# Kernel tuning notes

Measured on AMD Instinct MI355X. Metric: run time of the kernel, lower is better.

The kernel has to match this reference:

```python
import jax, jax.numpy as jnp
import numpy as np

E = 1024  # embed_dim
H = 16    # num_heads
D = E // H  # head_dim
B, S = 2, 2048

def _xavier(key, shape):
    fan_in, fan_out = shape[1], shape[0]
    limit = float(np.sqrt(6.0 / (fan_in + fan_out)))
    return jax.random.uniform(key, shape, jnp.float32, -limit, limit)

def setup_inputs() -> dict:
    key = jax.random.key(0)
    ks = jax.random.split(key, 7)
    return {
        "query": jax.random.normal(ks[0], (B, S, E), jnp.float32),
        "key": jax.random.normal(ks[1], (B, S, E), jnp.float32),
        "value": jax.random.normal(ks[2], (B, S, E), jnp.float32),
        "Wq": _xavier(ks[3], (E, E)), "bq": jnp.zeros((E,), jnp.float32),
        "Wk": _xavier(ks[4], (E, E)), "bk": jnp.zeros((E,), jnp.float32),
        "Wv": _xavier(ks[5], (E, E)), "bv": jnp.zeros((E,), jnp.float32),
        "Wo": _xavier(ks[6], (E, E)), "bo": jnp.zeros((E,), jnp.float32),
    }

def reference(query, key, value, Wq, bq, Wk, bk, Wv, bv, Wo, bo):
    b, s, e = query.shape
    # nn.Linear: x @ W^T + b
    Q = (query @ Wq.T + bq).reshape(b, s, H, D).transpose(0, 2, 1, 3)  # [b,h,s,d]
    K = (key @ Wk.T + bk).reshape(b, s, H, D).transpose(0, 2, 1, 3)
    V = (value @ Wv.T + bv).reshape(b, s, H, D).transpose(0, 2, 1, 3)
    scale = D ** -0.5
    scores = jnp.einsum('bhqd,bhkd->bhqk', Q, K) * scale  # [b,h,s,s]
    attn = jax.nn.softmax(scores, axis=-1)  # dropout=0.0 -> identity
    out = jnp.einsum('bhqk,bhkd->bhqd', attn, V)
    out = out.transpose(0, 2, 1, 3).reshape(b, s, e)
    return out @ Wo.T + bo
```

## Files before the change

kernel.cpp:

```cpp
#include <hip/hip_runtime.h>
#include <stdint.h>

#define E_DIM 1024
#define N_HEADS 16
#define HEAD_D 64
#define BATCH 2
#define SEQ 2048
#define M_ROWS (BATCH*SEQ)

typedef __attribute__((ext_vector_type(8))) short short8;
typedef __attribute__((ext_vector_type(4))) short short4_t;
typedef __attribute__((ext_vector_type(4))) float f32x4;
typedef __attribute__((ext_vector_type(4))) int i32x4;
typedef __attribute__((ext_vector_type(2))) int i32x2;

__device__ __forceinline__ unsigned short f2bf(float f) {
  uint32_t u = __float_as_uint(f);
  u += 0x7FFFu + ((u >> 16) & 1u);
  return (unsigned short)(u >> 16);
}

__device__ __forceinline__ void gload_lds16(const void* g, void* l) {
  __builtin_amdgcn_global_load_lds(
      (const __attribute__((address_space(1))) uint32_t*)(uintptr_t)g,
      (__attribute__((address_space(3))) uint32_t*)(uint32_t)(uintptr_t)l,
      16, 0, 0);
}

__device__ __forceinline__ int cvtpk(float lo, float hi) {
  int r;
  asm("v_cvt_pk_bf16_f32 %0, %1, %2" : "=v"(r) : "v"(lo), "v"(hi));
  return r;
}

__device__ __forceinline__ void cvt_body(const float* __restrict__ src,
                                         unsigned short* __restrict__ dst, int i) {
  f32x4 a = ((const f32x4*)src)[2*i];
  f32x4 b = ((const f32x4*)src)[2*i + 1];
  union { unsigned short us[8]; i32x4 v; } o;
  o.us[0] = f2bf(a[0]); o.us[1] = f2bf(a[1]);
  o.us[2] = f2bf(a[2]); o.us[3] = f2bf(a[3]);
  o.us[4] = f2bf(b[0]); o.us[5] = f2bf(b[1]);
  o.us[6] = f2bf(b[2]); o.us[7] = f2bf(b[3]);
  ((i32x4*)dst)[i] = o.v;
}

__global__ void cvt_all(const float* __restrict__ x0, const float* __restrict__ x1,
                        const float* __restrict__ x2,
                        const float* __restrict__ w0, const float* __restrict__ w1,
                        const float* __restrict__ w2, const float* __restrict__ w3,
                        unsigned short* __restrict__ dx0, unsigned short* __restrict__ dx1,
                        unsigned short* __restrict__ dx2,
                        unsigned short* __restrict__ dw0, unsigned short* __restrict__ dw1,
                        unsigned short* __restrict__ dw2, unsigned short* __restrict__ dw3) {
  const int i = blockIdx.x * blockDim.x + threadIdx.x;
  constexpr int NX8 = M_ROWS * E_DIM / 8;
  constexpr int NW8 = E_DIM * E_DIM / 8;
  if (i < 3 * NX8) {
    const int r = i >> 19, off = i & (NX8 - 1);
    const float* s = (r == 0) ? x0 : (r == 1) ? x1 : x2;
    unsigned short* d = (r == 0) ? dx0 : (r == 1) ? dx1 : dx2;
    cvt_body(s, d, off);
  } else {
    const int j = i - 3 * NX8;
    const int r = j >> 17, off = j & (NW8 - 1);
    const float* s = (r == 0) ? w0 : (r == 1) ? w1 : (r == 2) ? w2 : w3;
    unsigned short* d = (r == 0) ? dw0 : (r == 1) ? dw1 : (r == 2) ? dw2 : dw3;
    cvt_body(s, d, off);
  }
}

__device__ __forceinline__ void gemm_body_rt8(const unsigned short* __restrict__ A,
                                              const unsigned short* __restrict__ Bm,
                                              const float* __restrict__ bias,
                                              unsigned short* __restrict__ Cout,
                                              float scale, int bx, int by,
                                              int Nstr, bool brow) {
  constexpr int BM = 128, BN = 128, BK = 64, K = E_DIM;
  __shared__ __attribute__((aligned(16))) unsigned short Al[2][BM*BK];
  __shared__ __attribute__((aligned(16))) unsigned short Bl[2][BN*BK];
  const int tid  = threadIdx.x;
  const int lane = tid & 63, w = tid >> 6;
  const int wm = w >> 2, wn = w & 3;
  const int l15 = lane & 15, l4 = lane >> 4, l7 = lane & 7;
  const int m0 = by * BM, n0 = bx * BN;
  const int jr = lane >> 3, jc = lane & 7;
  const int kcg = jc ^ jr;

#define GSTAGE(KT, BUF)                                                        \
  do {                                                                         \
    _Pragma("unroll")                                                          \
    for (int t = 0; t < 2; ++t) {             \
      int ia = w*2 + t;                                                        \
      const char* src = (const char*)A +                                       \
          ((size_t)(m0 + ia*8 + jr)*K + (KT))*2 + (kcg << 4);                  \
      gload_lds16(src, (char*)Al[BUF] + ia*1024);                              \
    }                                                                          \
    _Pragma("unroll")                                                          \
    for (int t = 0; t < 2; ++t) {                    \
      int ib = w*2 + t;                                                        \
      const char* src = (const char*)Bm +                                      \
          ((size_t)(n0 + ib*8 + jr)*K + (KT))*2 + (kcg << 4);                  \
      gload_lds16(src, (char*)Bl[BUF] + ib*1024);                              \
    }                                                                          \
  } while (0)

  f32x4 zero = {0.f, 0.f, 0.f, 0.f};
  f32x4 acc[4][2];
  for (int i = 0; i < 4; ++i) for (int j = 0; j < 2; ++j) acc[i][j] = zero;

  GSTAGE(0, 0);
  __syncthreads();

  int cur = 0;
  const int NKT = K / BK;
  for (int kt = 0; kt < NKT; ++kt) {
    if (kt + 1 < NKT) GSTAGE((kt + 1) * BK, cur ^ 1);

#pragma unroll
    for (int ks = 0; ks < 2; ++ks) {
      const int sw = ((ks*4 + l4) ^ l7) << 4;
      short8 af[4], bf[2];
#pragma unroll
      for (int mf = 0; mf < 4; ++mf)
        af[mf] = *(const short8*)((const char*)Al[cur] + (wm*64 + mf*16 + l15)*128 + sw);
#pragma unroll
      for (int nf = 0; nf < 2; ++nf)
        bf[nf] = *(const short8*)((const char*)Bl[cur] + (wn*32 + nf*16 + l15)*128 + sw);
      __builtin_amdgcn_s_setprio(1);
#pragma unroll
      for (int mf = 0; mf < 4; ++mf)
#pragma unroll
        for (int nf = 0; nf < 2; ++nf)
          acc[mf][nf] = __builtin_amdgcn_mfma_f32_16x16x32_bf16(
              af[mf], bf[nf], acc[mf][nf], 0, 0, 0);
      __builtin_amdgcn_s_setprio(0);
    }

    __syncthreads();
    cur ^= 1;
  }
#undef GSTAGE

#pragma unroll
  for (int nf = 0; nf < 2; ++nf) {
    const int col = n0 + wn*32 + nf*16 + l15;
    const float bcol = brow ? 0.f : bias[col];
#pragma unroll
    for (int mf = 0; mf < 4; ++mf) {
      const int rowb = m0 + wm*64 + mf*16 + l4*4;
#pragma unroll
      for (int r = 0; r < 4; ++r) {
        const float bv = brow ? bias[rowb + r] : bcol;
        float v = (acc[mf][nf][r] + bv) * scale;
        Cout[(size_t)(rowb + r)*Nstr + col] = f2bf(v);
      }
    }
  }
}

__global__ __launch_bounds__(512, 4)
void gemm_qkv(const unsigned short* __restrict__ Xq, const unsigned short* __restrict__ Xk,
              const unsigned short* __restrict__ Xv,
              const unsigned short* __restrict__ Wq, const unsigned short* __restrict__ Wk,
              const unsigned short* __restrict__ Wv,
              const float* __restrict__ bq, const float* __restrict__ bk,
              const float* __restrict__ bv,
              unsigned short* __restrict__ Qb, unsigned short* __restrict__ Kb,
              unsigned short* __restrict__ Vt, float scale0) {
  const int z = blockIdx.z;
  const int idx = blockIdx.x;
  if (z == 2) {
    gemm_body_rt8(Wv, Xv, bv, Vt, 1.0f, idx & 31, idx >> 5, M_ROWS, true);
  } else {
    const unsigned short* A  = (z == 0) ? Xq : Xk;
    const unsigned short* Bm = (z == 0) ? Wq : Wk;
    const float* bias        = (z == 0) ? bq : bk;
    unsigned short* C        = (z == 0) ? Qb : Kb;
    const float scale        = (z == 0) ? scale0 : 1.0f;
    gemm_body_rt8(A, Bm, bias, C, scale, idx & 7, idx >> 3, E_DIM, false);
  }
}

__global__ __launch_bounds__(256, 2)
void gemm_o(const unsigned short* __restrict__ A, const unsigned short* __restrict__ Bm,
            const float* __restrict__ bias, float* __restrict__ Cout) {
  constexpr int BM = 128, BN = 64, BK = 64, K = E_DIM, N = E_DIM;
  __shared__ __attribute__((aligned(16))) unsigned short Al[2][BM*BK];
  __shared__ __attribute__((aligned(16))) unsigned short Bl[2][BN*BK];
  const int tid  = threadIdx.x;
  const int lane = tid & 63, w = tid >> 6;
  const int wm = w >> 1, wn = w & 1;
  const int l15 = lane & 15, l4 = lane >> 4, l7 = lane & 7;
  const int m0 = blockIdx.y * BM, n0 = blockIdx.x * BN;
  const int jr = lane >> 3, jc = lane & 7;
  const int kcg = jc ^ jr;

#define GSTAGE(KT, BUF)                                                        \
  do {                                                                         \
    _Pragma("unroll")                                                          \
    for (int t = 0; t < 4; ++t) {                                              \
      int ia = w*4 + t;                                                        \
      const char* src = (const char*)A +                                       \
          ((size_t)(m0 + ia*8 + jr)*K + (KT))*2 + (kcg << 4);                  \
      gload_lds16(src, (char*)Al[BUF] + ia*1024);                              \
    }                                                                          \
    _Pragma("unroll")                                                          \
    for (int t = 0; t < 2; ++t) {                                              \
      int ib = w*2 + t;                                                        \
      const char* src = (const char*)Bm +                                      \
          ((size_t)(n0 + ib*8 + jr)*K + (KT))*2 + (kcg << 4);                  \
      gload_lds16(src, (char*)Bl[BUF] + ib*1024);                              \
    }                                                                          \
  } while (0)

  f32x4 zero = {0.f, 0.f, 0.f, 0.f};
  f32x4 acc[4][2];
  for (int i = 0; i < 4; ++i) for (int j = 0; j < 2; ++j) acc[i][j] = zero;

  GSTAGE(0, 0);
  __syncthreads();

  int cur = 0;
  const int NKT = K / BK;
  for (int kt = 0; kt < NKT; ++kt) {
    if (kt + 1 < NKT) GSTAGE((kt + 1) * BK, cur ^ 1);
#pragma unroll
    for (int ks = 0; ks < 2; ++ks) {
      const int sw = ((ks*4 + l4) ^ l7) << 4;
      short8 af[4], bf[2];
#pragma unroll
      for (int mf = 0; mf < 4; ++mf)
        af[mf] = *(const short8*)((const char*)Al[cur] + (wm*64 + mf*16 + l15)*128 + sw);
#pragma unroll
      for (int nf = 0; nf < 2; ++nf)
        bf[nf] = *(const short8*)((const char*)Bl[cur] + (wn*32 + nf*16 + l15)*128 + sw);
      __builtin_amdgcn_s_setprio(1);
#pragma unroll
      for (int mf = 0; mf < 4; ++mf)
#pragma unroll
        for (int nf = 0; nf < 2; ++nf)
          acc[mf][nf] = __builtin_amdgcn_mfma_f32_16x16x32_bf16(
              af[mf], bf[nf], acc[mf][nf], 0, 0, 0);
      __builtin_amdgcn_s_setprio(0);
    }
    __syncthreads();
    cur ^= 1;
  }
#undef GSTAGE

#pragma unroll
  for (int nf = 0; nf < 2; ++nf) {
    const int col = n0 + wn*32 + nf*16 + l15;
    const float bv = bias[col];
#pragma unroll
    for (int mf = 0; mf < 4; ++mf) {
      const int rowb = m0 + wm*64 + mf*16 + l4*4;
#pragma unroll
      for (int r = 0; r < 4; ++r)
        Cout[(size_t)(rowb + r)*N + col] = acc[mf][nf][r] + bv;
    }
  }
}

__global__ __launch_bounds__(512, 2)
void attn_fwd6(const unsigned short* __restrict__ Q,
               const unsigned short* __restrict__ Kg,
               const unsigned short* __restrict__ Vt_g,
               unsigned short* __restrict__ O) {
  __shared__ __attribute__((aligned(16))) unsigned short Kl[2][4096];
  __shared__ __attribute__((aligned(16))) unsigned short Vl[2][4096];
  __shared__ __attribute__((aligned(16))) unsigned short Pl[8][1024];

  const int tid = threadIdx.x;
  const int l = tid & 63, w = tid >> 6;
  const int l15 = l & 15, l4 = l >> 4, l7 = l & 7;

  const int id = blockIdx.x;
  const int bh = (id & 7) * 4 + ((id >> 3) & 3);
  const int qt = id >> 5;
  const int b = bh >> 4, h = bh & 15;
  const size_t bS = (size_t)b * SEQ;
  const int qw = qt * 128 + w * 16;

  short8 qf[2];
  {
    const char* qp = (const char*)Q + ((bS + qw + l15) * E_DIM + h * 64) * 2;
    qf[0] = *(const short8*)(qp + l4 * 16);
    qf[1] = *(const short8*)(qp + 64 + l4 * 16);
  }

  f32x4 zero = {0.f, 0.f, 0.f, 0.f};
  f32x4 oacc[4];
#pragma unroll
  for (int i = 0; i < 4; ++i) oacc[i] = zero;
  float mrow = -1e30f, lrow = 0.f;

  const int krow = l >> 3;
  const int kcg  = (l & 7) ^ krow;
  const char* vt_base = (const char*)Vt_g +
      ((size_t)(h * 64 + 8 * w + krow) * M_ROWS + bS) * 2 + (kcg << 4);

#define KSTAGE(KT, BUF)                                                        \
  gload_lds16((const char*)Kg +                                                \
                  ((bS + (size_t)(KT)*64 + 8*w + krow) * E_DIM + h*64 + kcg*8)*2, \
              (char*)Kl[BUF] + w * 1024)

#define VSTAGE(KT, BUF)                                                        \
  gload_lds16(vt_base + (size_t)(KT) * 128, (char*)Vl[BUF] + w * 1024)

  KSTAGE(0, 0);
  VSTAGE(0, 0);
  __syncthreads();

  int cur = 0;
  constexpr int NT = SEQ / 64;
  for (int kt = 0; kt < NT; ++kt) {
    const bool more = (kt + 1 < NT);
    if (more) {
      KSTAGE(kt + 1, cur ^ 1);
      VSTAGE(kt + 1, cur ^ 1);
    }

    f32x4 s[4];
    const char* kb = (const char*)Kl[cur];
    __builtin_amdgcn_s_setprio(1);
#pragma unroll
    for (int nf = 0; nf < 4; ++nf) {
      const char* rowb = kb + (nf * 16 + l15) * 128;
      short8 k0 = *(const short8*)(rowb + ((l4 ^ l7) << 4));
      short8 k1 = *(const short8*)(rowb + (((4 + l4) ^ l7) << 4));
      f32x4 z = zero;
      z = __builtin_amdgcn_mfma_f32_16x16x32_bf16(k0, qf[0], z, 0, 0, 0);
      z = __builtin_amdgcn_mfma_f32_16x16x32_bf16(k1, qf[1], z, 0, 0, 0);
      s[nf] = z;
    }
    __builtin_amdgcn_s_setprio(0);

    float mx = s[0][0];
#pragma unroll
    for (int nf = 0; nf < 4; ++nf)
#pragma unroll
      for (int r = 0; r < 4; ++r) mx = fmaxf(mx, s[nf][r]);
    mx = fmaxf(mx, __shfl_xor(mx, 16));
    mx = fmaxf(mx, __shfl_xor(mx, 32));
    const float mnew = fmaxf(mrow, mx);
    const float fac = __builtin_amdgcn_exp2f(mrow - mnew);
    mrow = mnew;

    float pv[4][4];
    float rs = 0.f;
#pragma unroll
    for (int nf = 0; nf < 4; ++nf)
#pragma unroll
      for (int r = 0; r < 4; ++r) {
        float p = __builtin_amdgcn_exp2f(s[nf][r] - mnew);
        pv[nf][r] = p;
        rs += p;
      }
    rs += __shfl_xor(rs, 16);
    rs += __shfl_xor(rs, 32);
    lrow = lrow * fac + rs;

    unsigned short* pw = Pl[w];
#pragma unroll
    for (int nf = 0; nf < 4; ++nf) {
      const int c = nf * 2 + (l4 >> 1);
      i32x2 pk;
      pk.x = cvtpk(pv[nf][0], pv[nf][1]);
      pk.y = cvtpk(pv[nf][2], pv[nf][3]);
      *(i32x2*)((char*)pw + l15 * 128 + ((c ^ l7) << 4) + ((l4 & 1) << 3)) = pk;
    }
    short8 pf0 = *(const short8*)((const char*)pw + l15 * 128 + ((l4 ^ l7) << 4));
    short8 pf1 = *(const short8*)((const char*)pw + l15 * 128 + (((4 + l4) ^ l7) << 4));

#pragma unroll
    for (int df = 0; df < 4; ++df)
#pragma unroll
      for (int r = 0; r < 4; ++r) oacc[df][r] *= fac;

    const char* vb = (const char*)Vl[cur];
    __builtin_amdgcn_s_setprio(1);
#pragma unroll
    for (int df = 0; df < 4; ++df) {
      const char* rowb = vb + (df * 16 + l15) * 128;
      short8 v0 = *(const short8*)(rowb + ((l4 ^ l7) << 4));
      short8 v1 = *(const short8*)(rowb + (((4 + l4) ^ l7) << 4));
      oacc[df] = __builtin_amdgcn_mfma_f32_16x16x32_bf16(v0, pf0, oacc[df], 0, 0, 0);
      oacc[df] = __builtin_amdgcn_mfma_f32_16x16x32_bf16(v1, pf1, oacc[df], 0, 0, 0);
    }
    __builtin_amdgcn_s_setprio(0);

    __syncthreads();
    cur ^= 1;
  }
#undef KSTAGE
#undef VSTAGE

  const float rinv = __builtin_amdgcn_rcpf(lrow);
  unsigned short* orow = O + (bS + qw + l15) * E_DIM + h * 64;
#pragma unroll
  for (int df = 0; df < 4; ++df) {
    short4_t o4;
#pragma unroll
    for (int r = 0; r < 4; ++r) o4[r] = (short)f2bf(oacc[df][r] * rinv);
    *(short4_t*)(orow + df * 16 + l4 * 4) = o4;
  }
}

extern "C" void kernel_launch(void* const* d_in, const int* in_sizes, int n_in,
                              void* d_out, int out_size, void* d_ws, size_t ws_size,
                              hipStream_t stream) {
  const float* q_in = (const float*)d_in[0];
  const float* k_in = (const float*)d_in[1];
  const float* v_in = (const float*)d_in[2];
  const float* Wq = (const float*)d_in[3];
  const float* bq = (const float*)d_in[4];
  const float* Wk = (const float*)d_in[5];
  const float* bk = (const float*)d_in[6];
  const float* Wv = (const float*)d_in[7];
  const float* bv = (const float*)d_in[8];
  const float* Wo = (const float*)d_in[9];
  const float* bo = (const float*)d_in[10];

  char* ws = (char*)d_ws;
  const size_t XB = (size_t)M_ROWS * E_DIM * 2;
  const size_t WB = (size_t)E_DIM * E_DIM * 2;
  unsigned short* Xq  = (unsigned short*)(ws);
  unsigned short* Xk  = (unsigned short*)(ws + XB);
  unsigned short* Xv  = (unsigned short*)(ws + 2*XB);
  unsigned short* Wqb = (unsigned short*)(ws + 3*XB);
  unsigned short* Wkb = (unsigned short*)(ws + 3*XB + WB);
  unsigned short* Wvb = (unsigned short*)(ws + 3*XB + 2*WB);
  unsigned short* Wob = (unsigned short*)(ws + 3*XB + 3*WB);
  unsigned short* Qb  = (unsigned short*)(ws + 3*XB + 4*WB);
  unsigned short* Kb  = (unsigned short*)(ws + 4*XB + 4*WB);
  unsigned short* Vtg = (unsigned short*)(ws + 5*XB + 4*WB);
  unsigned short* Ob  = (unsigned short*)(ws + 6*XB + 4*WB);

  cvt_all<<<8192, 256, 0, stream>>>(q_in, k_in, v_in, Wq, Wk, Wv, Wo,
                                    Xq, Xk, Xv, Wqb, Wkb, Wvb, Wob);

  const float qscale = 0.125f * 1.44269504088896340736f;
  gemm_qkv<<<dim3(256, 1, 3), 512, 0, stream>>>(Xq, Xk, Xv, Wqb, Wkb, Wvb,
                                                bq, bk, bv, Qb, Kb, Vtg, qscale);

  attn_fwd6<<<512, 512, 0, stream>>>(Qb, Kb, Vtg, Ob);

  dim3 ogrid(E_DIM/64, M_ROWS/128);
  gemm_o<<<ogrid, 256, 0, stream>>>(Ob, Wob, bo, (float*)d_out);
}
```

Baseline: 122.3 us.

## Process two query sub-tiles per wave to reuse K/V fragments in attention

Each wave in the attention kernel now handles 32 query rows (two 16-row groups) instead of 16, so each block covers 256 queries and the grid is halved. K fragments are loaded from LDS once per tile and reused for both groups, and V fragments are shared across the two P·V MFMA chains. This cuts global K/V staging traffic and LDS reads per unit of work. In exchange, register pressure rises, the P scratch buffer doubles, and only 256 blocks launch, which lowers occupancy and latency hiding.

```diff
diff --git a/kernel.cpp b/kernel.cpp
--- a/kernel.cpp
+++ b/kernel.cpp
@@ -90,14 +90,14 @@
 #define GSTAGE(KT, BUF)                                                        \
   do {                                                                         \
     _Pragma("unroll")                                                          \
-    for (int t = 0; t < 2; ++t) {             \
+    for (int t = 0; t < 2; ++t) {                                              \
       int ia = w*2 + t;                                                        \
       const char* src = (const char*)A +                                       \
           ((size_t)(m0 + ia*8 + jr)*K + (KT))*2 + (kcg << 4);                  \
       gload_lds16(src, (char*)Al[BUF] + ia*1024);                              \
     }                                                                          \
     _Pragma("unroll")                                                          \
-    for (int t = 0; t < 2; ++t) {                    \
+    for (int t = 0; t < 2; ++t) {                                              \
       int ib = w*2 + t;                                                        \
       const char* src = (const char*)Bm +                                      \
           ((size_t)(n0 + ib*8 + jr)*K + (KT))*2 + (kcg << 4);                  \
@@ -264,13 +264,13 @@
 }
 
 __global__ __launch_bounds__(512, 2)
-void attn_fwd6(const unsigned short* __restrict__ Q,
+void attn_fwd7(const unsigned short* __restrict__ Q,
                const unsigned short* __restrict__ Kg,
                const unsigned short* __restrict__ Vt_g,
                unsigned short* __restrict__ O) {
   __shared__ __attribute__((aligned(16))) unsigned short Kl[2][4096];
   __shared__ __attribute__((aligned(16))) unsigned short Vl[2][4096];
-  __shared__ __attribute__((aligned(16))) unsigned short Pl[8][1024];
+  __shared__ __attribute__((aligned(16))) unsigned short Pl[8][2][1024];
 
   const int tid = threadIdx.x;
   const int l = tid & 63, w = tid >> 6;
@@ -281,20 +281,23 @@
   const int qt = id >> 5;
   const int b = bh >> 4, h = bh & 15;
   const size_t bS = (size_t)b * SEQ;
-  const int qw = qt * 128 + w * 16;
-
-  short8 qf[2];
-  {
-    const char* qp = (const char*)Q + ((bS + qw + l15) * E_DIM + h * 64) * 2;
-    qf[0] = *(const short8*)(qp + l4 * 16);
-    qf[1] = *(const short8*)(qp + 64 + l4 * 16);
+  const int qw = qt * 256 + w * 32;
+
+  short8 qf[2][2];
+#pragma unroll
+  for (int g = 0; g < 2; ++g) {
+    const char* qp = (const char*)Q + ((bS + qw + g*16 + l15) * E_DIM + h * 64) * 2;
+    qf[g][0] = *(const short8*)(qp + l4 * 16);
+    qf[g][1] = *(const short8*)(qp + 64 + l4 * 16);
   }
 
   f32x4 zero = {0.f, 0.f, 0.f, 0.f};
-  f32x4 oacc[4];
-#pragma unroll
-  for (int i = 0; i < 4; ++i) oacc[i] = zero;
-  float mrow = -1e30f, lrow = 0.f;
+  f32x4 oacc[2][4];
+#pragma unroll
+  for (int g = 0; g < 2; ++g)
+#pragma unroll
+    for (int i = 0; i < 4; ++i) oacc[g][i] = zero;
+  float mrow[2] = {-1e30f, -1e30f}, lrow[2] = {0.f, 0.f};
 
   const int krow = l >> 3;
   const int kcg  = (l & 7) ^ krow;
@@ -322,74 +325,90 @@
       VSTAGE(kt + 1, cur ^ 1);
     }
 
-    f32x4 s[4];
-    const char* kb = (const char*)Kl[cur];
-    __builtin_amdgcn_s_setprio(1);
-#pragma unroll
-    for (int nf = 0; nf < 4; ++nf) {
-      const char* rowb = kb + (nf * 16 + l15) * 128;
-      short8 k0 = *(const short8*)(rowb + ((l4 ^ l7) << 4));
-      short8 k1 = *(const short8*)(rowb + (((4 + l4) ^ l7) << 4));
-      f32x4 z = zero;
-      z = __builtin_amdgcn_mfma_f32_16x16x32_bf16(k0, qf[0], z, 0, 0, 0);
-      z = __builtin_amdgcn_mfma_f32_16x16x32_bf16(k1, qf[1], z, 0, 0, 0);
-      s[nf] = z;
-    }
-    __builtin_amdgcn_s_setprio(0);
-
-    float mx = s[0][0];
-#pragma unroll
-    for (int nf = 0; nf < 4; ++nf)
-#pragma unroll
-      for (int r = 0; r < 4; ++r) mx = fmaxf(mx, s[nf][r]);
-    mx = fmaxf(mx, __shfl_xor(mx, 16));
-    mx = fmaxf(mx, __shfl_xor(mx, 32));
-    const float mnew = fmaxf(mrow, mx);
-    const float fac = __builtin_amdgcn_exp2f(mrow - mnew);
-    mrow = mnew;
-
-    float pv[4][4];
-    float rs = 0.f;
-#pragma unroll
-    for (int nf = 0; nf < 4; ++nf)
-#pragma unroll
-      for (int r = 0; r < 4; ++r) {
-        float p = __builtin_amdgcn_exp2f(s[nf][r] - mnew);
-        pv[nf][r] = p;
-        rs += p;
+    short8 kf[8];
+    {
+      const char* kb = (const char*)Kl[cur];
+#pragma unroll
+      for (int nf = 0; nf < 4; ++nf) {
+        const char* rowb = kb + (nf * 16 + l15) * 128;
+        kf[nf*2]     = *(const short8*)(rowb + ((l4 ^ l7) << 4));
+        kf[nf*2 + 1] = *(const short8*)(rowb + (((4 + l4) ^ l7) << 4));
       }
-    rs += __shfl_xor(rs, 16);
-    rs += __shfl_xor(rs, 32);
-    lrow = lrow * fac + rs;
-
-    unsigned short* pw = Pl[w];
-#pragma unroll
-    for (int nf = 0; nf < 4; ++nf) {
-      const int c = nf * 2 + (l4 >> 1);
-      i32x2 pk;
-      pk.x = cvtpk(pv[nf][0], pv[nf][1]);
-      pk.y = cvtpk(pv[nf][2], pv[nf][3]);
-      *(i32x2*)((char*)pw + l15 * 128 + ((c ^ l7) << 4) + ((l4 & 1) << 3)) = pk;
-    }
-    short8 pf0 = *(const short8*)((const char*)pw + l15 * 128 + ((l4 ^ l7) << 4));
-    short8 pf1 = *(const short8*)((const char*)pw + l15 * 128 + (((4 + l4) ^ l7) << 4));
-
-#pragma unroll
-    for (int df = 0; df < 4; ++df)
-#pragma unroll
-      for (int r = 0; r < 4; ++r) oacc[df][r] *= fac;
-
-    const char* vb = (const char*)Vl[cur];
-    __builtin_amdgcn_s_setprio(1);
-#pragma unroll
-    for (int df = 0; df < 4; ++df) {
-      const char* rowb = vb + (df * 16 + l15) * 128;
-      short8 v0 = *(const short8*)(rowb + ((l4 ^ l7) << 4));
-      short8 v1 = *(const short8*)(rowb + (((4 + l4) ^ l7) << 4));
-      oacc[df] = __builtin_amdgcn_mfma_f32_16x16x32_bf16(v0, pf0, oacc[df], 0, 0, 0);
-      oacc[df] = __builtin_amdgcn_mfma_f32_16x16x32_bf16(v1, pf1, oacc[df], 0, 0, 0);
-    }
-    __builtin_amdgcn_s_setprio(0);
+    }
+
+    short8 pf[2][2];
+#pragma unroll
+    for (int g = 0; g < 2; ++g) {
+      f32x4 s[4];
+      __builtin_amdgcn_s_setprio(1);
+#pragma unroll
+      for (int nf = 0; nf < 4; ++nf) {
+        f32x4 z = zero;
+        z = __builtin_amdgcn_mfma_f32_16x16x32_bf16(kf[nf*2],     qf[g][0], z, 0, 0, 0);
+        z = __builtin_amdgcn_mfma_f32_16x16x32_bf16(kf[nf*2 + 1], qf[g][1], z, 0, 0, 0);
+        s[nf] = z;
+      }
+      __builtin_amdgcn_s_setprio(0);
+
+      float mx = s[0][0];
+#pragma unroll
+      for (int nf = 0; nf < 4; ++nf)
+#pragma unroll
+        for (int r = 0; r < 4; ++r) mx = fmaxf(mx, s[nf][r]);
+      mx = fmaxf(mx, __shfl_xor(mx, 16));
+      mx = fmaxf(mx, __shfl_xor(mx, 32));
+      const float mnew = fmaxf(mrow[g], mx);
+      const float fac = __builtin_amdgcn_exp2f(mrow[g] - mnew);
+      mrow[g] = mnew;
+
+      float pv[4][4];
+      float rs = 0.f;
+#pragma unroll
+      for (int nf = 0; nf < 4; ++nf)
+#pragma unroll
+        for (int r = 0; r < 4; ++r) {
+          float p = __builtin_amdgcn_exp2f(s[nf][r] - mnew);
+          pv[nf][r] = p;
+          rs += p;
+        }
+      rs += __shfl_xor(rs, 16);
+      rs += __shfl_xor(rs, 32);
+      lrow[g] = lrow[g] * fac + rs;
+
+#pragma unroll
+      for (int df = 0; df < 4; ++df)
+#pragma unroll
+        for (int r = 0; r < 4; ++r) oacc[g][df][r] *= fac;
+
+      char* pw = (char*)&Pl[w][g][0];
+#pragma unroll
+      for (int nf = 0; nf < 4; ++nf) {
+        const int c = nf * 2 + (l4 >> 1);
+        i32x2 pk;
+        pk.x = cvtpk(pv[nf][0], pv[nf][1]);
+        pk.y = cvtpk(pv[nf][2], pv[nf][3]);
+        *(i32x2*)(pw + l15 * 128 + ((c ^ l7) << 4) + ((l4 & 1) << 3)) = pk;
+      }
+      pf[g][0] = *(const short8*)(pw + l15 * 128 + ((l4 ^ l7) << 4));
+      pf[g][1] = *(const short8*)(pw + l15 * 128 + (((4 + l4) ^ l7) << 4));
+    }
+
+    {
+      const char* vbuf = (const char*)Vl[cur];
+      __builtin_amdgcn_s_setprio(1);
+#pragma unroll
+      for (int df = 0; df < 4; ++df) {
+        const char* rowb = vbuf + (df * 16 + l15) * 128;
+        short8 v0 = *(const short8*)(rowb + ((l4 ^ l7) << 4));
+        short8 v1 = *(const short8*)(rowb + (((4 + l4) ^ l7) << 4));
+#pragma unroll
+        for (int g = 0; g < 2; ++g) {
+          oacc[g][df] = __builtin_amdgcn_mfma_f32_16x16x32_bf16(v0, pf[g][0], oacc[g][df], 0, 0, 0);
+          oacc[g][df] = __builtin_amdgcn_mfma_f32_16x16x32_bf16(v1, pf[g][1], oacc[g][df], 0, 0, 0);
+        }
+      }
+      __builtin_amdgcn_s_setprio(0);
+    }
 
     __syncthreads();
     cur ^= 1;
@@ -397,14 +416,17 @@
 #undef KSTAGE
 #undef VSTAGE
 
-  const float rinv = __builtin_amdgcn_rcpf(lrow);
-  unsigned short* orow = O + (bS + qw + l15) * E_DIM + h * 64;
-#pragma unroll
-  for (int df = 0; df < 4; ++df) {
-    short4_t o4;
-#pragma unroll
-    for (int r = 0; r < 4; ++r) o4[r] = (short)f2bf(oacc[df][r] * rinv);
-    *(short4_t*)(orow + df * 16 + l4 * 4) = o4;
+#pragma unroll
+  for (int g = 0; g < 2; ++g) {
+    const float rinv = __builtin_amdgcn_rcpf(lrow[g]);
+    unsigned short* orow = O + (bS + qw + g*16 + l15) * E_DIM + h * 64;
+#pragma unroll
+    for (int df = 0; df < 4; ++df) {
+      short4_t o4;
+#pragma unroll
+      for (int r = 0; r < 4; ++r) o4[r] = (short)f2bf(oacc[g][df][r] * rinv);
+      *(short4_t*)(orow + df * 16 + l4 * 4) = o4;
+    }
   }
 }
 
@@ -445,7 +467,7 @@
   gemm_qkv<<<dim3(256, 1, 3), 512, 0, stream>>>(Xq, Xk, Xv, Wqb, Wkb, Wvb,
                                                 bq, bk, bv, Qb, Kb, Vtg, qscale);
 
-  attn_fwd6<<<512, 512, 0, stream>>>(Qb, Kb, Vtg, Ob);
+  attn_fwd7<<<256, 512, 0, stream>>>(Qb, Kb, Vtg, Ob);
 
   dim3 ogrid(E_DIM/64, M_ROWS/128);
   gemm_o<<<ogrid, 256, 0, stream>>>(Ob, Wob, bo, (float*)d_out);
```

After: 121.9 us. No clear change (-0.3%).
